# Performance work log

Hardware: AMD Instinct MI355X
Metric: run time of the kernel (lower is better)

Reference implementation:

```python
import jax, jax.numpy as jnp
import numpy as np

NUM_SAMPLES = 64
NUM_FINE_SAMPLES = 128
BATCH = 131072


def setup_inputs() -> dict:
    key = jax.random.key(0)
    k1, k2, k3, k4 = jax.random.split(key, 4)
    near = 0.5 + jax.random.uniform(k1, (BATCH, 1), dtype=jnp.float32)          # [0.5, 1.5]
    far = near + 2.0 + 4.0 * jax.random.uniform(k2, (BATCH, 1), dtype=jnp.float32)  # near + [2, 6]
    density = 5.0 * jax.random.uniform(k3, (BATCH, NUM_SAMPLES), dtype=jnp.float32)
    rgb = jax.random.uniform(k4, (BATCH, NUM_SAMPLES, 3), dtype=jnp.float32)
    return {"near": near, "far": far, "density": density, "rgb": rgb}


def _hierarchical_sample(bins, weights, num_samples):
    # bins, weights: [B, N]; deterministic u (pertube=False branch)
    B, N = weights.shape
    pdf = weights / (jnp.sum(weights, -1, keepdims=True) + 1e-6)
    cdf = jnp.cumsum(pdf, -1)                                   # [B, N]
    u = jnp.broadcast_to(jnp.linspace(0.05, 0.95, num_samples, dtype=bins.dtype), (B, num_samples))
    inds = jax.vmap(lambda c, uu: jnp.searchsorted(c, uu, side='right'))(cdf, u)  # [B, Nf]
    below = jnp.maximum(inds - 1, 0)
    above = jnp.minimum(inds, N - 1)
    cdf_b = jnp.take_along_axis(cdf, below, -1)
    cdf_a = jnp.take_along_axis(cdf, above, -1)
    bins_b = jnp.take_along_axis(bins, below, -1)
    bins_a = jnp.take_along_axis(bins, above, -1)
    denom = cdf_a - cdf_b
    denom = jnp.where(denom < 1e-5, jnp.ones_like(denom), denom)
    t = (u - cdf_b) / denom
    return bins_b + t * (bins_a - bins_b)                       # [B, Nf]


def reference(near, far, density, rgb):
    # --- coarse frustum (deterministic, pertub=False path of _sample_coarse_frustum) ---
    unit = jnp.linspace(0.0, 1.0, NUM_SAMPLES + 1, dtype=near.dtype)  # [N+1]
    zs_edges = near * (1.0 - unit) + far * unit                 # [B, N+1]
    start, end = zs_edges[:, :-1], zs_edges[:, 1:]
    deltas = end - start                                        # [B, N]
    mids = 0.5 * (start + end)                                  # frustum.zs, [B, N]

    # --- _compute_weight: alpha compositing transmittance ---
    alpha = 1.0 - jnp.exp(-density * deltas)                    # [B, N]
    trans = jnp.cumprod(jnp.concatenate([jnp.ones_like(alpha[:, :1]), 1.0 - alpha], -1), -1)[:, :-1]
    weight = alpha * trans                                      # [B, N]

    # --- _sample_fine_frustum: inverse-CDF sampling + merge-sort of zs ---
    fine_zs = _hierarchical_sample(mids, weight, NUM_FINE_SAMPLES)  # [B, Nf] (no_grad in original)
    fine_zs = jax.lax.stop_gradient(fine_zs)
    combined_zs = jnp.sort(jnp.concatenate([mids, fine_zs], -1), -1)  # [B, N+Nf]

    # --- volume_render of the coarse pass ---
    rgb_out = jnp.sum(weight[..., None] * rgb, axis=1)          # [B, 3]
    acc = jnp.sum(weight, -1, keepdims=True)                    # [B, 1]
    depth = jnp.sum(weight * mids, -1, keepdims=True) / (acc + 1e-8)  # normalized composite
    return combined_zs, rgb_out, depth, acc
```

## Files before the change

kernel.cpp:

```cpp
#include <hip/hip_runtime.h>

#define BATCH 131072
#define NS 64
#define NF 128
#define NTOT 192
#define WPB 4
#define RPW 4
#define RPB (WPB * RPW)
#define CDF_STRIDE 68
#define COMB_STRIDE 196

#define DPP_ADD_F(x, ctrl)                                                   \
    x += __int_as_float(__builtin_amdgcn_update_dpp(                         \
        0, __float_as_int(x), ctrl, 0xf, 0xf, true))
#define DPP_ADD_I(x, ctrl)                                                   \
    x += __builtin_amdgcn_update_dpp(0, x, ctrl, 0xf, 0xf, true)

__device__ __forceinline__ float row_iscan_f(float x) {
    DPP_ADD_F(x, 0x111);
    DPP_ADD_F(x, 0x112);
    DPP_ADD_F(x, 0x114);
    DPP_ADD_F(x, 0x118);
    return x;
}
__device__ __forceinline__ int row_iscan_i(int x) {
    DPP_ADD_I(x, 0x111);
    DPP_ADD_I(x, 0x112);
    DPP_ADD_I(x, 0x114);
    DPP_ADD_I(x, 0x118);
    return x;
}
__device__ __forceinline__ float row_bcast15_f(float x) {
    return __int_as_float(__builtin_amdgcn_ds_swizzle(__float_as_int(x), 0x1F0));
}

__global__ __launch_bounds__(256) void pdf_sampler_kernel(
    const float* __restrict__ near_p,
    const float* __restrict__ far_p,
    const float* __restrict__ density,
    const float* __restrict__ rgb,
    float* __restrict__ out)
{
    const int lane = threadIdx.x & 63;
    const int wave = threadIdx.x >> 6;
    const int g    = lane >> 4;
    const int j    = lane & 15;
    const int rayBase = (blockIdx.x * WPB + wave) * RPW;
    const int ray   = rayBase + g;
    const int rslot = (wave << 2) | g;

    __shared__ float s_cdf[RPB * CDF_STRIDE];
    __shared__ __align__(16) float s_comb[RPB * COMB_STRIDE];
    float* cdfb = s_cdf  + rslot * CDF_STRIDE;
    float* comb = s_comb + rslot * COMB_STRIDE;
    int*   hist = reinterpret_cast<int*>(comb);

    const float nearv = near_p[ray];
    const float farv  = far_p[ray];
    const float4 dv = *reinterpret_cast<const float4*>(
        &density[(size_t)rayBase * NS + 4 * lane]);
    const float4* rgbw = reinterpret_cast<const float4*>(
        &rgb[(size_t)rayBase * NS * 3]);
    const float4 c0 = rgbw[3 * lane + 0];
    const float4 c1 = rgbw[3 * lane + 1];
    const float4 c2 = rgbw[3 * lane + 2];

    const float Bc = (farv - nearv) * (1.0f / 64.0f);
    const float Ac = __fmaf_rn(0.5f, Bc, nearv);
    const int s0 = 4 * j;
    float mid[4];
    #pragma unroll
    for (int i = 0; i < 4; ++i) mid[i] = __fmaf_rn(Bc, (float)(s0 + i), Ac);

    const float q0 = dv.x;
    const float q1 = q0 + dv.y;
    const float q2 = q1 + dv.z;
    const float q3 = q2 + dv.w;
    const float rexq = row_iscan_f(q3) - q3;
    float e[4];
    e[0] = __expf(-Bc * (rexq + q0));
    e[1] = __expf(-Bc * (rexq + q1));
    e[2] = __expf(-Bc * (rexq + q2));
    e[3] = __expf(-Bc * (rexq + q3));
    const float eprev0 = __int_as_float(__builtin_amdgcn_update_dpp(
        0x3f800000, __float_as_int(e[3]), 0x111, 0xf, 0xf, false));
    const float w0 = eprev0 - e[0];
    const float w1 = e[0] - e[1];
    const float w2 = e[1] - e[2];
    const float w3 = e[2] - e[3];

    const float elast = row_bcast15_f(e[3]);
    const float wsum  = 1.0f - elast;
    const float rcpw  = __builtin_amdgcn_rcpf(wsum + 1e-6f);
    float cdf[4];
    #pragma unroll
    for (int i = 0; i < 4; ++i) cdf[i] = (1.0f - e[i]) * rcpw;

    *reinterpret_cast<float4*>(&cdfb[s0]) =
        make_float4(cdf[0], cdf[1], cdf[2], cdf[3]);
    int4* hz = reinterpret_cast<int4*>(hist);
    hz[2 * j + 0] = make_int4(0, 0, 0, 0);
    hz[2 * j + 1] = make_int4(0, 0, 0, 0);

    const float step = 0.9f / 127.0f;
    int t[4];
    #pragma unroll
    for (int i = 0; i < 4; ++i) {
        int tt = (int)ceilf((cdf[i] - 0.05f) * (127.0f / 0.9f));
        tt = tt < 0 ? 0 : (tt > 128 ? 128 : tt);
        if (tt > 0   && __fmaf_rn(step, (float)(tt - 1), 0.05f) >= cdf[i]) --tt;
        if (tt < 128 && __fmaf_rn(step, (float)tt,       0.05f) <  cdf[i]) ++tt;
        t[i] = tt;
    }

    __builtin_amdgcn_wave_barrier();
    #pragma unroll
    for (int i = 0; i < 4; ++i)
        if (t[i] < 128) atomicAdd(&hist[t[i]], 1);
    __builtin_amdgcn_wave_barrier();

    const float wr = row_iscan_f(__fmaf_rn(w0, c0.x, __fmaf_rn(w1, c0.w,
                     __fmaf_rn(w2, c1.z, w3 * c2.y))));
    const float wg = row_iscan_f(__fmaf_rn(w0, c0.y, __fmaf_rn(w1, c1.x,
                     __fmaf_rn(w2, c1.w, w3 * c2.z))));
    const float wb = row_iscan_f(__fmaf_rn(w0, c0.z, __fmaf_rn(w1, c1.y,
                     __fmaf_rn(w2, c2.x, w3 * c2.w))));
    const float wm = row_iscan_f(__fmaf_rn(w0, mid[0], __fmaf_rn(w1, mid[1],
                     __fmaf_rn(w2, mid[2], w3 * mid[3]))));
    if (j == 15) {
        float* rgb_out   = out + (size_t)BATCH * NTOT;
        float* depth_out = rgb_out + (size_t)BATCH * 3;
        float* acc_out   = depth_out + BATCH;
        rgb_out[ray * 3 + 0] = wr;
        rgb_out[ray * 3 + 1] = wg;
        rgb_out[ray * 3 + 2] = wb;
        depth_out[ray] = wm * __builtin_amdgcn_rcpf(wsum + 1e-8f);
        acc_out[ray]   = wsum;
    }

    int hv[8];
    {
        const int4 a = hz[2 * j + 0];
        const int4 b = hz[2 * j + 1];
        hv[0] = a.x; hv[1] = a.y; hv[2] = a.z; hv[3] = a.w;
        hv[4] = b.x; hv[5] = b.y; hv[6] = b.z; hv[7] = b.w;
    }
    __builtin_amdgcn_wave_barrier();
    int lp[8];
    {
        int a8 = 0;
        #pragma unroll
        for (int i = 0; i < 8; ++i) { a8 += hv[i]; lp[i] = a8; }
        const int ri = row_iscan_i(a8);
        const int re = ri - a8;
        #pragma unroll
        for (int i = 0; i < 8; ++i) lp[i] += re;
    }

    const float step2 = 0.9f / 127.0f;
    #pragma unroll
    for (int i = 0; i < 8; ++i) {
        const int k   = 8 * j + i;
        const int ind = lp[i];
        const int below = ind > 0 ? ind - 1 : 0;
        const int above = ind < NS - 1 ? ind : NS - 1;
        const float cb = cdfb[below];
        const float ca = cdfb[above];
        float denom = ca - cb;
        if (denom < 1e-5f) denom = 1.0f;
        const float u  = __fmaf_rn(step2, (float)k, 0.05f);
        const float tt = (u - cb) * __builtin_amdgcn_rcpf(denom);
        const float mb = __fmaf_rn(Bc, (float)below, Ac);
        const float dm = Bc * (float)(above - below);
        comb[k + below + 1] = __fmaf_rn(tt, dm, mb);
    }
    #pragma unroll
    for (int i = 0; i < 4; ++i) {
        const int s = s0 + i;
        comb[s ? s + t[i] : 0] = mid[i];
    }

    __builtin_amdgcn_wave_barrier();

    float* outw = out + (size_t)rayBase * NTOT;
    #pragma unroll
    for (int m = 0; m < 3; ++m) {
        const int f   = lane + 64 * m;
        const int r   = (f * 683) >> 15;
        const int off = f - 48 * r;
        const float4 v = *reinterpret_cast<const float4*>(
            &s_comb[((wave << 2) | r) * COMB_STRIDE + 4 * off]);
        reinterpret_cast<float4*>(outw)[f] = v;
    }
}

extern "C" void kernel_launch(void* const* d_in, const int* in_sizes, int n_in,
                              void* d_out, int out_size, void* d_ws, size_t ws_size,
                              hipStream_t stream) {
    const float* near_p  = (const float*)d_in[0];
    const float* far_p   = (const float*)d_in[1];
    const float* density = (const float*)d_in[2];
    const float* rgb     = (const float*)d_in[3];
    float* out = (float*)d_out;

    const int grid = BATCH / RPB;
    pdf_sampler_kernel<<<grid, 256, 0, stream>>>(near_p, far_p, density, rgb, out);
}
```

Before: 211.5 us.

## Use persistent grid with register prefetch of next ray group's inputs

The one-shot grid is replaced by a fixed grid of 2048 blocks. Each wave now loops over several ray groups and prefetches the next group's near/far/density/rgb into registers while it computes the current one. The aim is to hide global-load latency behind compute and to cut block launch overhead. In exchange, register pressure rises from holding the prefetched values, which may lower occupancy, and the smaller grid exposes less parallelism.

After: 215.5 us. About the same (+1.9%).

```diff
diff --git a/kernel.cpp b/kernel.cpp
--- a/kernel.cpp
+++ b/kernel.cpp
@@ -7,6 +7,8 @@
 #define WPB 4
 #define RPW 4
 #define RPB (WPB * RPW)
+#define GRID 2048
+#define ITERS (BATCH / (GRID * RPB))
 #define CDF_STRIDE 68
 #define COMB_STRIDE 196
 
@@ -45,9 +47,8 @@
     const int wave = threadIdx.x >> 6;
     const int g    = lane >> 4;
     const int j    = lane & 15;
-    const int rayBase = (blockIdx.x * WPB + wave) * RPW;
-    const int ray   = rayBase + g;
     const int rslot = (wave << 2) | g;
+    const int wgid  = blockIdx.x * WPB + wave;
 
     __shared__ float s_cdf[RPB * CDF_STRIDE];
     __shared__ __align__(16) float s_comb[RPB * COMB_STRIDE];
@@ -55,142 +56,169 @@
     float* comb = s_comb + rslot * COMB_STRIDE;
     int*   hist = reinterpret_cast<int*>(comb);
 
-    const float nearv = near_p[ray];
-    const float farv  = far_p[ray];
-    const float4 dv = *reinterpret_cast<const float4*>(
-        &density[(size_t)rayBase * NS + 4 * lane]);
-    const float4* rgbw = reinterpret_cast<const float4*>(
-        &rgb[(size_t)rayBase * NS * 3]);
-    const float4 c0 = rgbw[3 * lane + 0];
-    const float4 c1 = rgbw[3 * lane + 1];
-    const float4 c2 = rgbw[3 * lane + 2];
-
-    const float Bc = (farv - nearv) * (1.0f / 64.0f);
-    const float Ac = __fmaf_rn(0.5f, Bc, nearv);
-    const int s0 = 4 * j;
-    float mid[4];
+    int grp = wgid;
+    float nearv = near_p[grp * RPW + g];
+    float farv  = far_p[grp * RPW + g];
+    float4 dv = *reinterpret_cast<const float4*>(
+        &density[(size_t)grp * RPW * NS + 4 * lane]);
+    const float4* rgbw0 = reinterpret_cast<const float4*>(
+        &rgb[(size_t)grp * RPW * NS * 3]);
+    float4 c0 = rgbw0[3 * lane + 0];
+    float4 c1 = rgbw0[3 * lane + 1];
+    float4 c2 = rgbw0[3 * lane + 2];
+
     #pragma unroll
-    for (int i = 0; i < 4; ++i) mid[i] = __fmaf_rn(Bc, (float)(s0 + i), Ac);
-
-    const float q0 = dv.x;
-    const float q1 = q0 + dv.y;
-    const float q2 = q1 + dv.z;
-    const float q3 = q2 + dv.w;
-    const float rexq = row_iscan_f(q3) - q3;
-    float e[4];
-    e[0] = __expf(-Bc * (rexq + q0));
-    e[1] = __expf(-Bc * (rexq + q1));
-    e[2] = __expf(-Bc * (rexq + q2));
-    e[3] = __expf(-Bc * (rexq + q3));
-    const float eprev0 = __int_as_float(__builtin_amdgcn_update_dpp(
-        0x3f800000, __float_as_int(e[3]), 0x111, 0xf, 0xf, false));
-    const float w0 = eprev0 - e[0];
-    const float w1 = e[0] - e[1];
-    const float w2 = e[1] - e[2];
-    const float w3 = e[2] - e[3];
-
-    const float elast = row_bcast15_f(e[3]);
-    const float wsum  = 1.0f - elast;
-    const float rcpw  = __builtin_amdgcn_rcpf(wsum + 1e-6f);
-    float cdf[4];
-    #pragma unroll
-    for (int i = 0; i < 4; ++i) cdf[i] = (1.0f - e[i]) * rcpw;
-
-    *reinterpret_cast<float4*>(&cdfb[s0]) =
-        make_float4(cdf[0], cdf[1], cdf[2], cdf[3]);
-    int4* hz = reinterpret_cast<int4*>(hist);
-    hz[2 * j + 0] = make_int4(0, 0, 0, 0);
-    hz[2 * j + 1] = make_int4(0, 0, 0, 0);
-
-    const float step = 0.9f / 127.0f;
-    int t[4];
-    #pragma unroll
-    for (int i = 0; i < 4; ++i) {
-        int tt = (int)ceilf((cdf[i] - 0.05f) * (127.0f / 0.9f));
-        tt = tt < 0 ? 0 : (tt > 128 ? 128 : tt);
-        if (tt > 0   && __fmaf_rn(step, (float)(tt - 1), 0.05f) >= cdf[i]) --tt;
-        if (tt < 128 && __fmaf_rn(step, (float)tt,       0.05f) <  cdf[i]) ++tt;
-        t[i] = tt;
-    }
-
-    __builtin_amdgcn_wave_barrier();
-    #pragma unroll
-    for (int i = 0; i < 4; ++i)
-        if (t[i] < 128) atomicAdd(&hist[t[i]], 1);
-    __builtin_amdgcn_wave_barrier();
-
-    const float wr = row_iscan_f(__fmaf_rn(w0, c0.x, __fmaf_rn(w1, c0.w,
-                     __fmaf_rn(w2, c1.z, w3 * c2.y))));
-    const float wg = row_iscan_f(__fmaf_rn(w0, c0.y, __fmaf_rn(w1, c1.x,
-                     __fmaf_rn(w2, c1.w, w3 * c2.z))));
-    const float wb = row_iscan_f(__fmaf_rn(w0, c0.z, __fmaf_rn(w1, c1.y,
-                     __fmaf_rn(w2, c2.x, w3 * c2.w))));
-    const float wm = row_iscan_f(__fmaf_rn(w0, mid[0], __fmaf_rn(w1, mid[1],
-                     __fmaf_rn(w2, mid[2], w3 * mid[3]))));
-    if (j == 15) {
-        float* rgb_out   = out + (size_t)BATCH * NTOT;
-        float* depth_out = rgb_out + (size_t)BATCH * 3;
-        float* acc_out   = depth_out + BATCH;
-        rgb_out[ray * 3 + 0] = wr;
-        rgb_out[ray * 3 + 1] = wg;
-        rgb_out[ray * 3 + 2] = wb;
-        depth_out[ray] = wm * __builtin_amdgcn_rcpf(wsum + 1e-8f);
-        acc_out[ray]   = wsum;
-    }
-
-    int hv[8];
-    {
-        const int4 a = hz[2 * j + 0];
-        const int4 b = hz[2 * j + 1];
-        hv[0] = a.x; hv[1] = a.y; hv[2] = a.z; hv[3] = a.w;
-        hv[4] = b.x; hv[5] = b.y; hv[6] = b.z; hv[7] = b.w;
-    }
-    __builtin_amdgcn_wave_barrier();
-    int lp[8];
-    {
-        int a8 = 0;
-        #pragma unroll
-        for (int i = 0; i < 8; ++i) { a8 += hv[i]; lp[i] = a8; }
-        const int ri = row_iscan_i(a8);
-        const int re = ri - a8;
-        #pragma unroll
-        for (int i = 0; i < 8; ++i) lp[i] += re;
-    }
-
-    const float step2 = 0.9f / 127.0f;
-    #pragma unroll
-    for (int i = 0; i < 8; ++i) {
-        const int k   = 8 * j + i;
-        const int ind = lp[i];
-        const int below = ind > 0 ? ind - 1 : 0;
-        const int above = ind < NS - 1 ? ind : NS - 1;
-        const float cb = cdfb[below];
-        const float ca = cdfb[above];
-        float denom = ca - cb;
-        if (denom < 1e-5f) denom = 1.0f;
-        const float u  = __fmaf_rn(step2, (float)k, 0.05f);
-        const float tt = (u - cb) * __builtin_amdgcn_rcpf(denom);
-        const float mb = __fmaf_rn(Bc, (float)below, Ac);
-        const float dm = Bc * (float)(above - below);
-        comb[k + below + 1] = __fmaf_rn(tt, dm, mb);
-    }
-    #pragma unroll
-    for (int i = 0; i < 4; ++i) {
-        const int s = s0 + i;
-        comb[s ? s + t[i] : 0] = mid[i];
-    }
-
-    __builtin_amdgcn_wave_barrier();
-
-    float* outw = out + (size_t)rayBase * NTOT;
-    #pragma unroll
-    for (int m = 0; m < 3; ++m) {
-        const int f   = lane + 64 * m;
-        const int r   = (f * 683) >> 15;
-        const int off = f - 48 * r;
-        const float4 v = *reinterpret_cast<const float4*>(
-            &s_comb[((wave << 2) | r) * COMB_STRIDE + 4 * off]);
-        reinterpret_cast<float4*>(outw)[f] = v;
+    for (int it = 0; it < ITERS; ++it) {
+        const int rayBase = grp * RPW;
+        const int ray     = rayBase + g;
+
+        float nnear = 0.0f, nfar = 0.0f;
+        float4 ndv = {}, nc0 = {}, nc1 = {}, nc2 = {};
+        const int ngrp = grp + GRID * WPB;
+        if (it + 1 < ITERS) {
+            nnear = near_p[ngrp * RPW + g];
+            nfar  = far_p[ngrp * RPW + g];
+            ndv = *reinterpret_cast<const float4*>(
+                &density[(size_t)ngrp * RPW * NS + 4 * lane]);
+            const float4* rgbwn = reinterpret_cast<const float4*>(
+                &rgb[(size_t)ngrp * RPW * NS * 3]);
+            nc0 = rgbwn[3 * lane + 0];
+            nc1 = rgbwn[3 * lane + 1];
+            nc2 = rgbwn[3 * lane + 2];
+        }
+
+        const float Bc = (farv - nearv) * (1.0f / 64.0f);
+        const float Ac = __fmaf_rn(0.5f, Bc, nearv);
+        const int s0 = 4 * j;
+        float mid[4];
+        #pragma unroll
+        for (int i = 0; i < 4; ++i) mid[i] = __fmaf_rn(Bc, (float)(s0 + i), Ac);
+
+        const float q0 = dv.x;
+        const float q1 = q0 + dv.y;
+        const float q2 = q1 + dv.z;
+        const float q3 = q2 + dv.w;
+        const float rexq = row_iscan_f(q3) - q3;
+        float e[4];
+        e[0] = __expf(-Bc * (rexq + q0));
+        e[1] = __expf(-Bc * (rexq + q1));
+        e[2] = __expf(-Bc * (rexq + q2));
+        e[3] = __expf(-Bc * (rexq + q3));
+        const float eprev0 = __int_as_float(__builtin_amdgcn_update_dpp(
+            0x3f800000, __float_as_int(e[3]), 0x111, 0xf, 0xf, false));
+        const float w0 = eprev0 - e[0];
+        const float w1 = e[0] - e[1];
+        const float w2 = e[1] - e[2];
+        const float w3 = e[2] - e[3];
+
+        const float elast = row_bcast15_f(e[3]);
+        const float wsum  = 1.0f - elast;
+        const float rcpw  = __builtin_amdgcn_rcpf(wsum + 1e-6f);
+        float cdf[4];
+        #pragma unroll
+        for (int i = 0; i < 4; ++i) cdf[i] = (1.0f - e[i]) * rcpw;
+
+        *reinterpret_cast<float4*>(&cdfb[s0]) =
+            make_float4(cdf[0], cdf[1], cdf[2], cdf[3]);
+        int4* hz = reinterpret_cast<int4*>(hist);
+        hz[2 * j + 0] = make_int4(0, 0, 0, 0);
+        hz[2 * j + 1] = make_int4(0, 0, 0, 0);
+
+        const float step = 0.9f / 127.0f;
+        int t[4];
+        #pragma unroll
+        for (int i = 0; i < 4; ++i) {
+            int tt = (int)ceilf((cdf[i] - 0.05f) * (127.0f / 0.9f));
+            tt = tt < 0 ? 0 : (tt > 128 ? 128 : tt);
+            if (tt > 0   && __fmaf_rn(step, (float)(tt - 1), 0.05f) >= cdf[i]) --tt;
+            if (tt < 128 && __fmaf_rn(step, (float)tt,       0.05f) <  cdf[i]) ++tt;
+            t[i] = tt;
+        }
+
+        __builtin_amdgcn_wave_barrier();
+        #pragma unroll
+        for (int i = 0; i < 4; ++i)
+            if (t[i] < 128) atomicAdd(&hist[t[i]], 1);
+        __builtin_amdgcn_wave_barrier();
+
+        const float wr = row_iscan_f(__fmaf_rn(w0, c0.x, __fmaf_rn(w1, c0.w,
+                         __fmaf_rn(w2, c1.z, w3 * c2.y))));
+        const float wg = row_iscan_f(__fmaf_rn(w0, c0.y, __fmaf_rn(w1, c1.x,
+                         __fmaf_rn(w2, c1.w, w3 * c2.z))));
+        const float wb = row_iscan_f(__fmaf_rn(w0, c0.z, __fmaf_rn(w1, c1.y,
+                         __fmaf_rn(w2, c2.x, w3 * c2.w))));
+        const float wm = row_iscan_f(__fmaf_rn(w0, mid[0], __fmaf_rn(w1, mid[1],
+                         __fmaf_rn(w2, mid[2], w3 * mid[3]))));
+        if (j == 15) {
+            float* rgb_out   = out + (size_t)BATCH * NTOT;
+            float* depth_out = rgb_out + (size_t)BATCH * 3;
+            float* acc_out   = depth_out + BATCH;
+            rgb_out[ray * 3 + 0] = wr;
+            rgb_out[ray * 3 + 1] = wg;
+            rgb_out[ray * 3 + 2] = wb;
+            depth_out[ray] = wm * __builtin_amdgcn_rcpf(wsum + 1e-8f);
+            acc_out[ray]   = wsum;
+        }
+
+        int hv[8];
+        {
+            const int4 a = hz[2 * j + 0];
+            const int4 b = hz[2 * j + 1];
+            hv[0] = a.x; hv[1] = a.y; hv[2] = a.z; hv[3] = a.w;
+            hv[4] = b.x; hv[5] = b.y; hv[6] = b.z; hv[7] = b.w;
+        }
+        __builtin_amdgcn_wave_barrier();
+        int lp[8];
+        {
+            int a8 = 0;
+            #pragma unroll
+            for (int i = 0; i < 8; ++i) { a8 += hv[i]; lp[i] = a8; }
+            const int ri = row_iscan_i(a8);
+            const int re = ri - a8;
+            #pragma unroll
+            for (int i = 0; i < 8; ++i) lp[i] += re;
+        }
+
+        #pragma unroll
+        for (int i = 0; i < 8; ++i) {
+            const int k   = 8 * j + i;
+            const int ind = lp[i];
+            const int below = ind > 0 ? ind - 1 : 0;
+            const int above = ind < NS - 1 ? ind : NS - 1;
+            const float cb = cdfb[below];
+            const float ca = cdfb[above];
+            float denom = ca - cb;
+            if (denom < 1e-5f) denom = 1.0f;
+            const float u  = __fmaf_rn(step, (float)k, 0.05f);
+            const float tt = (u - cb) * __builtin_amdgcn_rcpf(denom);
+            const float mb = __fmaf_rn(Bc, (float)below, Ac);
+            const float dm = Bc * (float)(above - below);
+            comb[k + below + 1] = __fmaf_rn(tt, dm, mb);
+        }
+        #pragma unroll
+        for (int i = 0; i < 4; ++i) {
+            const int s = s0 + i;
+            comb[s ? s + t[i] : 0] = mid[i];
+        }
+
+        __builtin_amdgcn_wave_barrier();
+
+        float* outw = out + (size_t)rayBase * NTOT;
+        #pragma unroll
+        for (int m = 0; m < 3; ++m) {
+            const int f   = lane + 64 * m;
+            const int r   = (f * 683) >> 15;
+            const int off = f - 48 * r;
+            const float4 v = *reinterpret_cast<const float4*>(
+                &s_comb[((wave << 2) | r) * COMB_STRIDE + 4 * off]);
+            reinterpret_cast<float4*>(outw)[f] = v;
+        }
+
+        __builtin_amdgcn_wave_barrier();
+
+        nearv = nnear; farv = nfar;
+        dv = ndv; c0 = nc0; c1 = nc1; c2 = nc2;
+        grp = ngrp;
     }
 }
 
@@ -203,6 +231,5 @@
     const float* rgb     = (const float*)d_in[3];
     float* out = (float*)d_out;
 
-    const int grid = BATCH / RPB;
-    pdf_sampler_kernel<<<grid, 256, 0, stream>>>(near_p, far_p, density, rgb, out);
-}
+    pdf_sampler_kernel<<<GRID, 256, 0, stream>>>(near_p, far_p, density, rgb, out);
+}
```

## Process two ray groups per wave and reuse comb buffer for CDF

Applied to the files above, without the earlier changes.

Each wave now handles two groups of four rays instead of one, interleaving their loads, scans and sampling to raise memory-level and instruction-level parallelism per wave. The separate shared CDF array is removed; the CDF is stored in the tail of each ray's combined-zs buffer, and the fine-sample results are held in registers and written only after a barrier so they do not overwrite the CDF while it is being read. This raises register pressure and halves the grid size.

Result: no change. 213.5 us (+0.9%).

```diff
diff --git a/kernel.cpp b/kernel.cpp
--- a/kernel.cpp
+++ b/kernel.cpp
@@ -5,9 +5,10 @@
 #define NF 128
 #define NTOT 192
 #define WPB 4
-#define RPW 4
-#define RPB (WPB * RPW)
-#define CDF_STRIDE 68
+#define GPW 2
+#define RPG 4
+#define RPWAVE (GPW * RPG)
+#define RPB (WPB * RPWAVE)
 #define COMB_STRIDE 196
 
 #define DPP_ADD_F(x, ctrl)                                                   \
@@ -45,152 +46,194 @@
     const int wave = threadIdx.x >> 6;
     const int g    = lane >> 4;
     const int j    = lane & 15;
-    const int rayBase = (blockIdx.x * WPB + wave) * RPW;
-    const int ray   = rayBase + g;
-    const int rslot = (wave << 2) | g;
-
-    __shared__ float s_cdf[RPB * CDF_STRIDE];
+    const int s0   = 4 * j;
+    const int rayBase = (blockIdx.x * WPB + wave) * RPWAVE;
+
     __shared__ __align__(16) float s_comb[RPB * COMB_STRIDE];
-    float* cdfb = s_cdf  + rslot * CDF_STRIDE;
-    float* comb = s_comb + rslot * COMB_STRIDE;
-    int*   hist = reinterpret_cast<int*>(comb);
-
-    const float nearv = near_p[ray];
-    const float farv  = far_p[ray];
-    const float4 dv = *reinterpret_cast<const float4*>(
-        &density[(size_t)rayBase * NS + 4 * lane]);
-    const float4* rgbw = reinterpret_cast<const float4*>(
-        &rgb[(size_t)rayBase * NS * 3]);
-    const float4 c0 = rgbw[3 * lane + 0];
-    const float4 c1 = rgbw[3 * lane + 1];
-    const float4 c2 = rgbw[3 * lane + 2];
-
-    const float Bc = (farv - nearv) * (1.0f / 64.0f);
-    const float Ac = __fmaf_rn(0.5f, Bc, nearv);
-    const int s0 = 4 * j;
-    float mid[4];
-    #pragma unroll
-    for (int i = 0; i < 4; ++i) mid[i] = __fmaf_rn(Bc, (float)(s0 + i), Ac);
-
-    const float q0 = dv.x;
-    const float q1 = q0 + dv.y;
-    const float q2 = q1 + dv.z;
-    const float q3 = q2 + dv.w;
-    const float rexq = row_iscan_f(q3) - q3;
-    float e[4];
-    e[0] = __expf(-Bc * (rexq + q0));
-    e[1] = __expf(-Bc * (rexq + q1));
-    e[2] = __expf(-Bc * (rexq + q2));
-    e[3] = __expf(-Bc * (rexq + q3));
-    const float eprev0 = __int_as_float(__builtin_amdgcn_update_dpp(
-        0x3f800000, __float_as_int(e[3]), 0x111, 0xf, 0xf, false));
-    const float w0 = eprev0 - e[0];
-    const float w1 = e[0] - e[1];
-    const float w2 = e[1] - e[2];
-    const float w3 = e[2] - e[3];
-
-    const float elast = row_bcast15_f(e[3]);
-    const float wsum  = 1.0f - elast;
-    const float rcpw  = __builtin_amdgcn_rcpf(wsum + 1e-6f);
-    float cdf[4];
-    #pragma unroll
-    for (int i = 0; i < 4; ++i) cdf[i] = (1.0f - e[i]) * rcpw;
-
-    *reinterpret_cast<float4*>(&cdfb[s0]) =
-        make_float4(cdf[0], cdf[1], cdf[2], cdf[3]);
-    int4* hz = reinterpret_cast<int4*>(hist);
-    hz[2 * j + 0] = make_int4(0, 0, 0, 0);
-    hz[2 * j + 1] = make_int4(0, 0, 0, 0);
+
+    float* comb[GPW]; int* hist[GPW]; float* cdfb[GPW];
+    #pragma unroll
+    for (int p = 0; p < GPW; ++p) {
+        const int rslot = wave * RPWAVE + p * RPG + g;
+        comb[p] = s_comb + rslot * COMB_STRIDE;
+        hist[p] = reinterpret_cast<int*>(comb[p]);
+        cdfb[p] = comb[p] + 128;
+    }
+
+    float nearv[GPW], farv[GPW];
+    float4 dv[GPW], c0[GPW], c1[GPW], c2[GPW];
+    #pragma unroll
+    for (int p = 0; p < GPW; ++p) {
+        const int rb = rayBase + p * RPG;
+        nearv[p] = near_p[rb + g];
+        farv[p]  = far_p[rb + g];
+        dv[p] = *reinterpret_cast<const float4*>(
+            &density[(size_t)rb * NS + 4 * lane]);
+        const float4* rw = reinterpret_cast<const float4*>(
+            &rgb[(size_t)rb * NS * 3]);
+        c0[p] = rw[3 * lane + 0];
+        c1[p] = rw[3 * lane + 1];
+        c2[p] = rw[3 * lane + 2];
+    }
+
+    float Bc[GPW], Ac[GPW], wsum[GPW];
+    float mid[GPW][4], w_[GPW][4], cdf[GPW][4];
+    #pragma unroll
+    for (int p = 0; p < GPW; ++p) {
+        Bc[p] = (farv[p] - nearv[p]) * (1.0f / 64.0f);
+        Ac[p] = __fmaf_rn(0.5f, Bc[p], nearv[p]);
+        #pragma unroll
+        for (int i = 0; i < 4; ++i)
+            mid[p][i] = __fmaf_rn(Bc[p], (float)(s0 + i), Ac[p]);
+        const float q0 = dv[p].x;
+        const float q1 = q0 + dv[p].y;
+        const float q2 = q1 + dv[p].z;
+        const float q3 = q2 + dv[p].w;
+        const float rexq = row_iscan_f(q3) - q3;
+        float e0 = __expf(-Bc[p] * (rexq + q0));
+        float e1 = __expf(-Bc[p] * (rexq + q1));
+        float e2 = __expf(-Bc[p] * (rexq + q2));
+        float e3 = __expf(-Bc[p] * (rexq + q3));
+        const float eprev0 = __int_as_float(__builtin_amdgcn_update_dpp(
+            0x3f800000, __float_as_int(e3), 0x111, 0xf, 0xf, false));
+        w_[p][0] = eprev0 - e0;
+        w_[p][1] = e0 - e1;
+        w_[p][2] = e1 - e2;
+        w_[p][3] = e2 - e3;
+        const float elast = row_bcast15_f(e3);
+        wsum[p] = 1.0f - elast;
+        const float rcpw = __builtin_amdgcn_rcpf(wsum[p] + 1e-6f);
+        cdf[p][0] = (1.0f - e0) * rcpw;
+        cdf[p][1] = (1.0f - e1) * rcpw;
+        cdf[p][2] = (1.0f - e2) * rcpw;
+        cdf[p][3] = (1.0f - e3) * rcpw;
+    }
+
+    #pragma unroll
+    for (int p = 0; p < GPW; ++p) {
+        *reinterpret_cast<float4*>(&cdfb[p][s0]) =
+            make_float4(cdf[p][0], cdf[p][1], cdf[p][2], cdf[p][3]);
+        int4* hz = reinterpret_cast<int4*>(hist[p]);
+        hz[2 * j + 0] = make_int4(0, 0, 0, 0);
+        hz[2 * j + 1] = make_int4(0, 0, 0, 0);
+    }
 
     const float step = 0.9f / 127.0f;
-    int t[4];
-    #pragma unroll
-    for (int i = 0; i < 4; ++i) {
-        int tt = (int)ceilf((cdf[i] - 0.05f) * (127.0f / 0.9f));
-        tt = tt < 0 ? 0 : (tt > 128 ? 128 : tt);
-        if (tt > 0   && __fmaf_rn(step, (float)(tt - 1), 0.05f) >= cdf[i]) --tt;
-        if (tt < 128 && __fmaf_rn(step, (float)tt,       0.05f) <  cdf[i]) ++tt;
-        t[i] = tt;
-    }
-
-    __builtin_amdgcn_wave_barrier();
-    #pragma unroll
-    for (int i = 0; i < 4; ++i)
-        if (t[i] < 128) atomicAdd(&hist[t[i]], 1);
-    __builtin_amdgcn_wave_barrier();
-
-    const float wr = row_iscan_f(__fmaf_rn(w0, c0.x, __fmaf_rn(w1, c0.w,
-                     __fmaf_rn(w2, c1.z, w3 * c2.y))));
-    const float wg = row_iscan_f(__fmaf_rn(w0, c0.y, __fmaf_rn(w1, c1.x,
-                     __fmaf_rn(w2, c1.w, w3 * c2.z))));
-    const float wb = row_iscan_f(__fmaf_rn(w0, c0.z, __fmaf_rn(w1, c1.y,
-                     __fmaf_rn(w2, c2.x, w3 * c2.w))));
-    const float wm = row_iscan_f(__fmaf_rn(w0, mid[0], __fmaf_rn(w1, mid[1],
-                     __fmaf_rn(w2, mid[2], w3 * mid[3]))));
-    if (j == 15) {
-        float* rgb_out   = out + (size_t)BATCH * NTOT;
-        float* depth_out = rgb_out + (size_t)BATCH * 3;
-        float* acc_out   = depth_out + BATCH;
-        rgb_out[ray * 3 + 0] = wr;
-        rgb_out[ray * 3 + 1] = wg;
-        rgb_out[ray * 3 + 2] = wb;
-        depth_out[ray] = wm * __builtin_amdgcn_rcpf(wsum + 1e-8f);
-        acc_out[ray]   = wsum;
-    }
-
-    int hv[8];
-    {
+    int t[GPW][4];
+    #pragma unroll
+    for (int p = 0; p < GPW; ++p) {
+        #pragma unroll
+        for (int i = 0; i < 4; ++i) {
+            int tt = (int)ceilf((cdf[p][i] - 0.05f) * (127.0f / 0.9f));
+            tt = tt < 0 ? 0 : (tt > 128 ? 128 : tt);
+            if (tt > 0   && __fmaf_rn(step, (float)(tt - 1), 0.05f) >= cdf[p][i]) --tt;
+            if (tt < 128 && __fmaf_rn(step, (float)tt,       0.05f) <  cdf[p][i]) ++tt;
+            t[p][i] = tt;
+        }
+    }
+
+    __builtin_amdgcn_wave_barrier();
+    #pragma unroll
+    for (int p = 0; p < GPW; ++p)
+        #pragma unroll
+        for (int i = 0; i < 4; ++i)
+            if (t[p][i] < 128) atomicAdd(&hist[p][t[p][i]], 1);
+    __builtin_amdgcn_wave_barrier();
+
+    #pragma unroll
+    for (int p = 0; p < GPW; ++p) {
+        const float wr = row_iscan_f(__fmaf_rn(w_[p][0], c0[p].x,
+            __fmaf_rn(w_[p][1], c0[p].w, __fmaf_rn(w_[p][2], c1[p].z,
+            w_[p][3] * c2[p].y))));
+        const float wg = row_iscan_f(__fmaf_rn(w_[p][0], c0[p].y,
+            __fmaf_rn(w_[p][1], c1[p].x, __fmaf_rn(w_[p][2], c1[p].w,
+            w_[p][3] * c2[p].z))));
+        const float wb = row_iscan_f(__fmaf_rn(w_[p][0], c0[p].z,
+            __fmaf_rn(w_[p][1], c1[p].y, __fmaf_rn(w_[p][2], c2[p].x,
+            w_[p][3] * c2[p].w))));
+        const float wm = row_iscan_f(__fmaf_rn(w_[p][0], mid[p][0],
+            __fmaf_rn(w_[p][1], mid[p][1], __fmaf_rn(w_[p][2], mid[p][2],
+            w_[p][3] * mid[p][3]))));
+        if (j == 15) {
+            const int ray = rayBase + p * RPG + g;
+            float* rgb_out   = out + (size_t)BATCH * NTOT;
+            float* depth_out = rgb_out + (size_t)BATCH * 3;
+            float* acc_out   = depth_out + BATCH;
+            rgb_out[ray * 3 + 0] = wr;
+            rgb_out[ray * 3 + 1] = wg;
+            rgb_out[ray * 3 + 2] = wb;
+            depth_out[ray] = wm * __builtin_amdgcn_rcpf(wsum[p] + 1e-8f);
+            acc_out[ray]   = wsum[p];
+        }
+    }
+
+    int lp[GPW][8];
+    #pragma unroll
+    for (int p = 0; p < GPW; ++p) {
+        const int4* hz = reinterpret_cast<const int4*>(hist[p]);
         const int4 a = hz[2 * j + 0];
         const int4 b = hz[2 * j + 1];
-        hv[0] = a.x; hv[1] = a.y; hv[2] = a.z; hv[3] = a.w;
-        hv[4] = b.x; hv[5] = b.y; hv[6] = b.z; hv[7] = b.w;
-    }
-    __builtin_amdgcn_wave_barrier();
-    int lp[8];
-    {
+        int hv[8] = {a.x, a.y, a.z, a.w, b.x, b.y, b.z, b.w};
         int a8 = 0;
         #pragma unroll
-        for (int i = 0; i < 8; ++i) { a8 += hv[i]; lp[i] = a8; }
+        for (int i = 0; i < 8; ++i) { a8 += hv[i]; lp[p][i] = a8; }
         const int ri = row_iscan_i(a8);
         const int re = ri - a8;
         #pragma unroll
-        for (int i = 0; i < 8; ++i) lp[i] += re;
-    }
-
-    const float step2 = 0.9f / 127.0f;
-    #pragma unroll
-    for (int i = 0; i < 8; ++i) {
-        const int k   = 8 * j + i;
-        const int ind = lp[i];
-        const int below = ind > 0 ? ind - 1 : 0;
-        const int above = ind < NS - 1 ? ind : NS - 1;
-        const float cb = cdfb[below];
-        const float ca = cdfb[above];
-        float denom = ca - cb;
-        if (denom < 1e-5f) denom = 1.0f;
-        const float u  = __fmaf_rn(step2, (float)k, 0.05f);
-        const float tt = (u - cb) * __builtin_amdgcn_rcpf(denom);
-        const float mb = __fmaf_rn(Bc, (float)below, Ac);
-        const float dm = Bc * (float)(above - below);
-        comb[k + below + 1] = __fmaf_rn(tt, dm, mb);
-    }
-    #pragma unroll
-    for (int i = 0; i < 4; ++i) {
-        const int s = s0 + i;
-        comb[s ? s + t[i] : 0] = mid[i];
-    }
-
-    __builtin_amdgcn_wave_barrier();
-
-    float* outw = out + (size_t)rayBase * NTOT;
-    #pragma unroll
-    for (int m = 0; m < 3; ++m) {
-        const int f   = lane + 64 * m;
-        const int r   = (f * 683) >> 15;
-        const int off = f - 48 * r;
-        const float4 v = *reinterpret_cast<const float4*>(
-            &s_comb[((wave << 2) | r) * COMB_STRIDE + 4 * off]);
-        reinterpret_cast<float4*>(outw)[f] = v;
+        for (int i = 0; i < 8; ++i) lp[p][i] += re;
+    }
+
+    float fv[GPW][8];
+    int   ps[GPW][8];
+    #pragma unroll
+    for (int p = 0; p < GPW; ++p) {
+        #pragma unroll
+        for (int i = 0; i < 8; ++i) {
+            const int k   = 8 * j + i;
+            const int ind = lp[p][i];
+            const int below = ind > 0 ? ind - 1 : 0;
+            const int above = ind < NS - 1 ? ind : NS - 1;
+            const float cb = cdfb[p][below];
+            const float ca = cdfb[p][above];
+            float denom = ca - cb;
+            if (denom < 1e-5f) denom = 1.0f;
+            const float u  = __fmaf_rn(step, (float)k, 0.05f);
+            const float tt = (u - cb) * __builtin_amdgcn_rcpf(denom);
+            const float mb = __fmaf_rn(Bc[p], (float)below, Ac[p]);
+            const float dm = Bc[p] * (float)(above - below);
+            fv[p][i] = __fmaf_rn(tt, dm, mb);
+            ps[p][i] = k + below + 1;
+        }
+    }
+
+    __builtin_amdgcn_wave_barrier();
+
+    #pragma unroll
+    for (int p = 0; p < GPW; ++p) {
+        #pragma unroll
+        for (int i = 0; i < 8; ++i)
+            comb[p][ps[p][i]] = fv[p][i];
+        #pragma unroll
+        for (int i = 0; i < 4; ++i) {
+            const int s = s0 + i;
+            comb[p][s ? s + t[p][i] : 0] = mid[p][i];
+        }
+    }
+
+    __builtin_amdgcn_wave_barrier();
+
+    #pragma unroll
+    for (int p = 0; p < GPW; ++p) {
+        float* outw = out + (size_t)(rayBase + p * RPG) * NTOT;
+        #pragma unroll
+        for (int m = 0; m < 3; ++m) {
+            const int f   = lane + 64 * m;
+            const int r   = (f * 683) >> 15;
+            const int off = f - 48 * r;
+            const float4 v = *reinterpret_cast<const float4*>(
+                &s_comb[(wave * RPWAVE + p * RPG + r) * COMB_STRIDE + 4 * off]);
+            reinterpret_cast<float4*>(outw)[f] = v;
+        }
     }
 }
 
```
